# Kernel tuning notes

Measured on AMD Instinct MI355X. Metric: run time of the kernel, lower is better.

The kernel has to match this reference:

```python
import jax, jax.numpy as jnp
import numpy as np

B, S, D = 4, 4096, 256


def setup_inputs() -> dict:
    key = jax.random.key(0)
    ks = jax.random.split(key, 7)
    s = 1.0 / np.sqrt(D)
    return {
        "x": jax.random.normal(ks[0], (B, S, D), dtype=jnp.float32),
        "Wq": jax.random.uniform(ks[1], (D, D), jnp.float32, -s, s),
        "bq": jax.random.uniform(ks[2], (D,), jnp.float32, -s, s),
        "Wk": jax.random.uniform(ks[3], (D, D), jnp.float32, -s, s),
        "bk": jax.random.uniform(ks[4], (D,), jnp.float32, -s, s),
        "Wv": jax.random.uniform(ks[5], (D, D), jnp.float32, -s, s),
        "bv": jax.random.uniform(ks[6], (D,), jnp.float32, -s, s),
    }


def reference(x, Wq, bq, Wk, bk, Wv, bv):
    # nn.Linear: y = x @ W.T + b
    Q = jnp.einsum("bsd,ed->bse", x, Wq) + bq
    K = jnp.einsum("bsd,ed->bse", x, Wk) + bk
    V = jnp.einsum("bsd,ed->bse", x, Wv) + bv
    dk = Q.shape[-1]
    scores = jnp.einsum("bqd,bkd->bqk", Q, K) / jnp.sqrt(jnp.float32(dk))
    # NOTE: original applies softmax over dim=1 (the query axis), not -1.
    attn = jax.nn.softmax(scores, axis=1)
    out = jnp.einsum("bqk,bkd->bqd", attn, V)
    return out
```

## Files before the change

kernel.cpp:

```cpp
#include <hip/hip_runtime.h>

typedef short bf16x8 __attribute__((ext_vector_type(8)));
typedef float f32x4 __attribute__((ext_vector_type(4)));
typedef unsigned short u16;

#define S_LEN 4096
#define D_DIM 256
#define NROW  16384

__device__ __forceinline__ u16 f2bf(float f) {
    union { float f; unsigned u; } v; v.f = f;
    unsigned r = v.u + 0x7FFFu + ((v.u >> 16) & 1u);
    return (u16)(r >> 16);
}
__device__ __forceinline__ float bf2f(u16 h) {
    union { unsigned u; float f; } v; v.u = ((unsigned)h) << 16; return v.f;
}

__device__ __forceinline__ size_t fr_qk(int t, int kk) {
    return (size_t)t * 4096 + kk * 512;
}
__device__ __forceinline__ size_t fr_v(int p, int dt, int kk2) {
    return (size_t)p * 16384 + (dt * 2 + kk2) * 512;
}
__device__ __forceinline__ size_t e_base(int b, int kc, int qt) {
    return ((size_t)(b * 32768 + kc * 256 + qt)) * 512;
}

__device__ __forceinline__ void gll16(const u16* g, u16* l) {
    __builtin_amdgcn_global_load_lds(
        (const __attribute__((address_space(1))) unsigned int*)g,
        (__attribute__((address_space(3))) unsigned int*)l, 16, 0, 0);
}

#define WAITV6 asm volatile("s_waitcnt vmcnt(6)" ::: "memory")
#define WAITV4 asm volatile("s_waitcnt vmcnt(4)" ::: "memory")
#define WAITV0 asm volatile("s_waitcnt vmcnt(0)" ::: "memory")
#define WAITLGKM0 asm volatile("s_waitcnt lgkmcnt(0)" ::: "memory")
#define MEMFENCE asm volatile("" ::: "memory")

__global__ __launch_bounds__(256) void wconv(
    const float* __restrict__ Wq, const float* __restrict__ Wk,
    const float* __restrict__ Wv, u16* __restrict__ Wf)
{
    int i = blockIdx.x * 256 + threadIdx.x;
    int m = i >> 13;
    int idx = i & 8191;
    int ocol = idx >> 5;
    int d0 = (idx & 31) * 8;
    const float* s = (m == 0 ? Wq : (m == 1 ? Wk : Wv)) + ocol * 256 + d0;
    float4 v0 = *reinterpret_cast<const float4*>(s);
    float4 v1 = *reinterpret_cast<const float4*>(s + 4);
    union { ushort4 h[2]; int4 q; } t;
    t.h[0] = make_ushort4(f2bf(v0.x), f2bf(v0.y), f2bf(v0.z), f2bf(v0.w));
    t.h[1] = make_ushort4(f2bf(v1.x), f2bf(v1.y), f2bf(v1.z), f2bf(v1.w));
    size_t off = (size_t)m * 65536 + fr_qk(ocol >> 4, d0 >> 5)
               + ((d0 >> 3) & 3) * 128 + (ocol & 15) * 8;
    *reinterpret_cast<int4*>(Wf + off) = t.q;
}

__global__ __launch_bounds__(256) void qkv_proj(
    const float* __restrict__ x, const u16* __restrict__ Wf,
    const float* __restrict__ bq, const float* __restrict__ bk,
    const float* __restrict__ bv,
    u16* __restrict__ Qf, u16* __restrict__ Kf, u16* __restrict__ Vf)
{
    __shared__ u16 xs[32][264];
    const int tid = threadIdx.x;
    const int r0 = blockIdx.x * 32;

    #pragma unroll
    for (int i = 0; i < 8; ++i) {
        int c = i * 256 + tid;
        int row = c >> 6, c4 = c & 63;
        float4 v = reinterpret_cast<const float4*>(x + (size_t)(r0 + row) * D_DIM)[c4];
        *reinterpret_cast<ushort4*>(&xs[row][c4 * 4]) =
            make_ushort4(f2bf(v.x), f2bf(v.y), f2bf(v.z), f2bf(v.w));
    }
    __syncthreads();

    const int w = tid >> 6, l = tid & 63, lr = l & 15, lg = l >> 4;
    const int c0 = w * 64;

    bf16x8 a[2][8];
    #pragma unroll
    for (int qs = 0; qs < 2; ++qs)
        #pragma unroll
        for (int kk = 0; kk < 8; ++kk)
            a[qs][kk] = *reinterpret_cast<const bf16x8*>(&xs[qs * 16 + lr][kk * 32 + lg * 8]);

    const float* Bs[3] = {bq, bk, bv};

    #pragma unroll
    for (int m = 0; m < 3; ++m) {
        const u16* Wm = Wf + (size_t)m * 65536;
        f32x4 acc[2][4] = {};
        #pragma unroll
        for (int kk = 0; kk < 8; ++kk) {
            #pragma unroll
            for (int cf = 0; cf < 4; ++cf) {
                bf16x8 wfr = *reinterpret_cast<const bf16x8*>(
                    Wm + fr_qk(w * 4 + cf, kk) + l * 8);
                acc[0][cf] = __builtin_amdgcn_mfma_f32_16x16x32_bf16(a[0][kk], wfr, acc[0][cf], 0, 0, 0);
                acc[1][cf] = __builtin_amdgcn_mfma_f32_16x16x32_bf16(a[1][kk], wfr, acc[1][cf], 0, 0, 0);
            }
        }
        if (m < 2) {
            u16* outp = (m == 0) ? Qf : Kf;
            int t = r0 >> 4;
            #pragma unroll
            for (int qs = 0; qs < 2; ++qs) {
                #pragma unroll
                for (int cf = 0; cf < 4; ++cf) {
                    int col = c0 + cf * 16 + lr;
                    float bias = Bs[m][col];
                    size_t base = fr_qk(t + qs, col >> 5) + ((col >> 3) & 3) * 128 + (col & 7);
                    #pragma unroll
                    for (int r = 0; r < 4; ++r)
                        outp[base + (lg * 4 + r) * 8] = f2bf(acc[qs][cf][r] + bias);
                }
            }
        } else {
            int p  = (r0 >> 12) * 64 + ((r0 & 4095) >> 6);
            int kb = r0 & 63;
            #pragma unroll
            for (int qs = 0; qs < 2; ++qs) {
                #pragma unroll
                for (int cf = 0; cf < 4; ++cf) {
                    int d = c0 + cf * 16 + lr;
                    float bias = bv[d];
                    #pragma unroll
                    for (int r = 0; r < 4; ++r) {
                        int key = kb + qs * 16 + lg * 4 + r;
                        size_t off = fr_v(p, d >> 4, key >> 5)
                                   + ((key >> 3) & 3) * 128 + (d & 15) * 8 + (key & 7);
                        Vf[off] = f2bf(acc[qs][cf][r] + bias);
                    }
                }
            }
        }
    }
}

__global__ __launch_bounds__(256, 2) void score_exp(
    const u16* __restrict__ Qf, const u16* __restrict__ Kf,
    u16* __restrict__ Ef, float* __restrict__ Zp, int write_e)
{
    __shared__ __align__(16) u16 Qls[2][8192];
    const int tid = threadIdx.x, blk = blockIdx.x;
    const int xcd = blk & 7, sub = blk >> 3;
    const int b  = xcd >> 1;
    const int qq = ((xcd & 1) << 1) | (sub & 1);
    const int ktile = sub >> 1;
    const int w = tid >> 6, l = tid & 63, lr = l & 15, lg = l >> 4;
    const int k0 = ktile * 128;

    bf16x8 kreg[2][8];
    #pragma unroll
    for (int ks = 0; ks < 2; ++ks) {
        const int tk = b * 256 + (k0 >> 4) + w * 2 + ks;
        #pragma unroll
        for (int kk = 0; kk < 8; ++kk)
            kreg[ks][kk] = *reinterpret_cast<const bf16x8*>(Kf + fr_qk(tk, kk) + l * 8);
    }

    #define STAGE_Q(qt_, nb_) do { \
        const u16* g_ = Qf + ((size_t)(b * 256 + (qt_) * 2)) * 4096 + (w * 4) * 512 + l * 8; \
        u16* d_ = &Qls[nb_][(w * 4) * 512]; \
        _Pragma("unroll") \
        for (int f_ = 0; f_ < 4; ++f_) gll16(g_ + f_ * 512, d_ + f_ * 512); \
    } while (0)

    const int qt0 = qq * 32;
    STAGE_Q(qt0, 0);
    __syncthreads();

    float Z[2][4] = {};
    const float SC = 0.0625f;
    const int kc = ktile * 4 + w;

    for (int it = 0; it < 32; ++it) {
        const int cur = it & 1;
        if (it < 31) STAGE_Q(qt0 + it + 1, cur ^ 1);

        f32x4 acc[2][2] = {};
        #pragma unroll
        for (int kk = 0; kk < 8; ++kk) {
            #pragma unroll
            for (int qf = 0; qf < 2; ++qf) {
                bf16x8 qfr = *reinterpret_cast<const bf16x8*>(
                    &Qls[cur][(qf * 8 + kk) * 512 + l * 8]);
                acc[0][qf] = __builtin_amdgcn_mfma_f32_16x16x32_bf16(kreg[0][kk], qfr, acc[0][qf], 0, 0, 0);
                acc[1][qf] = __builtin_amdgcn_mfma_f32_16x16x32_bf16(kreg[1][kk], qfr, acc[1][qf], 0, 0, 0);
            }
        }
        #pragma unroll
        for (int ks = 0; ks < 2; ++ks) {
            #pragma unroll
            for (int qf = 0; qf < 2; ++qf) {
                float e0 = __expf(acc[ks][qf][0] * SC);
                float e1 = __expf(acc[ks][qf][1] * SC);
                float e2 = __expf(acc[ks][qf][2] * SC);
                float e3 = __expf(acc[ks][qf][3] * SC);
                Z[ks][0] += e0; Z[ks][1] += e1; Z[ks][2] += e2; Z[ks][3] += e3;
                if (write_e) {
                    size_t ad = e_base(b, kc, (qt0 + it) * 2 + qf)
                              + (ks * 2 + (lg >> 1)) * 128 + lr * 8 + (lg & 1) * 4;
                    *reinterpret_cast<ushort4*>(Ef + ad) =
                        make_ushort4(f2bf(e0), f2bf(e1), f2bf(e2), f2bf(e3));
                }
            }
        }
        __syncthreads();
    }

    #pragma unroll
    for (int ks = 0; ks < 2; ++ks) {
        #pragma unroll
        for (int r = 0; r < 4; ++r) {
            float z = Z[ks][r];
            z += __shfl_xor(z, 1);
            z += __shfl_xor(z, 2);
            z += __shfl_xor(z, 4);
            z += __shfl_xor(z, 8);
            if (lr == 0)
                Zp[qq * NROW + b * S_LEN + k0 + w * 32 + ks * 16 + lg * 4 + r] = z;
        }
    }
    #undef STAGE_Q
}

__global__ __launch_bounds__(256) void zrecip(
    const float* __restrict__ Zp, float* __restrict__ rZ)
{
    int i = blockIdx.x * 256 + threadIdx.x;
    rZ[i] = 1.0f / (((Zp[i] + Zp[NROW + i]) + Zp[2 * NROW + i]) + Zp[3 * NROW + i]);
}

__global__ __launch_bounds__(256) void zlog(
    const float* __restrict__ Zp, float* __restrict__ LZ)
{
    int i = blockIdx.x * 256 + threadIdx.x;
    LZ[i] = logf(((Zp[i] + Zp[NROW + i]) + Zp[2 * NROW + i]) + Zp[3 * NROW + i]);
}

__global__ __launch_bounds__(256) void vscale(
    u16* __restrict__ Vf, const float* __restrict__ rZ)
{
    int i = blockIdx.x * 256 + threadIdx.x;
    int frag = i >> 6, l8 = i & 63;
    int p = frag >> 5, sub = frag & 31, kk2 = sub & 1;
    int b = p >> 6, kt = p & 63;
    int kbase = b * S_LEN + kt * 64 + kk2 * 32 + (l8 >> 4) * 8;
    float4 rz0 = *reinterpret_cast<const float4*>(&rZ[kbase]);
    float4 rz1 = *reinterpret_cast<const float4*>(&rZ[kbase + 4]);
    ushort4* vp = reinterpret_cast<ushort4*>(Vf + (size_t)i * 8);
    ushort4 a = vp[0], c = vp[1];
    vp[0] = make_ushort4(f2bf(bf2f(a.x) * rz0.x), f2bf(bf2f(a.y) * rz0.y),
                         f2bf(bf2f(a.z) * rz0.z), f2bf(bf2f(a.w) * rz0.w));
    vp[1] = make_ushort4(f2bf(bf2f(c.x) * rz1.x), f2bf(bf2f(c.y) * rz1.y),
                         f2bf(bf2f(c.z) * rz1.z), f2bf(bf2f(c.w) * rz1.w));
}

__global__ __launch_bounds__(256, 2) void pv_gemm(
    const u16* __restrict__ Ef, const u16* __restrict__ Vf, float* __restrict__ out)
{
    __shared__ __align__(16) u16 Els[3][4096];
    __shared__ __align__(16) u16 Vls[3][8192];

    const int tid = threadIdx.x, blk = blockIdx.x;
    const int xcd = blk & 7, sub = blk >> 3;
    const int b  = xcd >> 1;
    const int kq = ((xcd & 1) << 1) | (sub & 1);
    const int qtile = sub >> 1;
    const int w = tid >> 6, l = tid & 63, lr = l & 15, lg = l >> 4;

    #define STAGE(it_) do { \
        const int kc_ = kq * 32 + (it_); \
        const int nb_ = (it_) % 3; \
        const size_t vb_ = ((size_t)(b * 64 + (kc_ >> 1))) * 16384 + (kc_ & 1) * 512; \
        _Pragma("unroll") \
        for (int i_ = 0; i_ < 6; ++i_) { \
            int f_ = w * 6 + i_; \
            if (f_ < 8) { \
                gll16(Ef + e_base(b, kc_, qtile * 8 + f_) + l * 8, &Els[nb_][f_ * 512]); \
            } else { \
                int dt_ = f_ - 8; \
                gll16(Vf + vb_ + (size_t)dt_ * 1024 + l * 8, &Vls[nb_][dt_ * 512]); \
            } \
        } \
    } while (0)

    STAGE(0);
    STAGE(1);
    WAITV6;
    __builtin_amdgcn_s_barrier();
    MEMFENCE;

    f32x4 acc[2][16] = {};

    #pragma unroll 1
    for (int it = 0; it < 32; ++it) {
        if (it < 30) STAGE(it + 2);
        const int cur = it % 3;
        bf16x8 ef0 = *reinterpret_cast<const bf16x8*>(&Els[cur][(w * 2) * 512 + l * 8]);
        bf16x8 ef1 = *reinterpret_cast<const bf16x8*>(&Els[cur][(w * 2 + 1) * 512 + l * 8]);
        __builtin_amdgcn_s_setprio(1);
        #pragma unroll
        for (int dt = 0; dt < 16; ++dt) {
            bf16x8 vfr = *reinterpret_cast<const bf16x8*>(&Vls[cur][dt * 512 + l * 8]);
            acc[0][dt] = __builtin_amdgcn_mfma_f32_16x16x32_bf16(ef0, vfr, acc[0][dt], 0, 0, 0);
            acc[1][dt] = __builtin_amdgcn_mfma_f32_16x16x32_bf16(ef1, vfr, acc[1][dt], 0, 0, 0);
        }
        __builtin_amdgcn_s_setprio(0);
        if (it < 30) { WAITV6; } else if (it == 30) { WAITV0; }
        if (it < 31) {
            __builtin_amdgcn_s_barrier();
            MEMFENCE;
        }
    }

    const int qg = b * S_LEN + qtile * 128 + w * 32;
    #pragma unroll
    for (int qs = 0; qs < 2; ++qs) {
        #pragma unroll
        for (int dt = 0; dt < 16; ++dt) {
            #pragma unroll
            for (int r = 0; r < 4; ++r) {
                unsafeAtomicAdd(&out[(size_t)(qg + qs * 16 + lg * 4 + r) * D_DIM + dt * 16 + lr],
                                acc[qs][dt][r]);
            }
        }
    }
    #undef STAGE
}

__global__ __launch_bounds__(512, 1) void attn_out_fb(
    const u16* __restrict__ Qf, const u16* __restrict__ Kf, const u16* __restrict__ Vf,
    const float* __restrict__ LZ, float* __restrict__ out)
{
    __shared__ __align__(16) u16 Kls[3][8192];
    __shared__ __align__(16) u16 Vls[4][8192];
    __shared__ __align__(16) u16 ps[8][2][1280];
    __shared__ __align__(16) float lzs[1024];

    const int tid = threadIdx.x, blk = blockIdx.x;
    const int xcd = blk & 7, sub = blk >> 3;
    const int b  = xcd >> 1;
    const int kq = ((xcd & 1) << 1) | (sub & 1);
    const int qtile = sub >> 1;
    const int w = tid >> 6, l = tid & 63, lr = l & 15, lg = l >> 4;
    const int q0 = qtile * 256 + w * 32;
    const int base_tk = b * 256;
    const int kt0 = kq * 32;

    bf16x8 qreg[2][8];
    #pragma unroll
    for (int qs = 0; qs < 2; ++qs) {
        const int tq = base_tk + ((q0 + qs * 16) >> 4);
        #pragma unroll
        for (int kk = 0; kk < 8; ++kk)
            qreg[qs][kk] = *reinterpret_cast<const bf16x8*>(Qf + fr_qk(tq, kk) + l * 8);
    }

    #define STAGE(kt_) do { \
        if (w < 4) { \
            const u16* g_ = Kf + ((size_t)(base_tk + (kt0 + (kt_)) * 2)) * 4096 + (w * 4) * 512 + l * 8; \
            u16* d_ = &Kls[(kt_) % 3][(w * 4) * 512]; \
            _Pragma("unroll") \
            for (int f_ = 0; f_ < 4; ++f_) gll16(g_ + f_ * 512, d_ + f_ * 512); \
        } else { \
            const int kta_ = kt0 + (kt_); \
            const size_t vb_ = ((size_t)(b * 64 + (kta_ >> 1))) * 16384 + (kta_ & 1) * 512; \
            const int dt0_ = (w - 4) * 4; \
            _Pragma("unroll") \
            for (int f_ = 0; f_ < 4; ++f_) \
                gll16(Vf + vb_ + (size_t)(dt0_ + f_) * 1024 + l * 8, &Vls[(kt_) % 4][(dt0_ + f_) * 512]); \
        } \
    } while (0)

    #define QK(kt_) do { \
        const u16* kb_ = &Kls[(kt_) % 3][0]; \
        __builtin_amdgcn_s_setprio(1); \
        _Pragma("unroll") \
        for (int kk = 0; kk < 8; ++kk) { \
            bf16x8 k0_ = *reinterpret_cast<const bf16x8*>(kb_ + kk * 512 + l * 8); \
            bf16x8 k1_ = *reinterpret_cast<const bf16x8*>(kb_ + (8 + kk) * 512 + l * 8); \
            sacc[0][0] = __builtin_amdgcn_mfma_f32_16x16x32_bf16(qreg[0][kk], k0_, sacc[0][0], 0, 0, 0); \
            sacc[0][1] = __builtin_amdgcn_mfma_f32_16x16x32_bf16(qreg[1][kk], k0_, sacc[0][1], 0, 0, 0); \
            sacc[1][0] = __builtin_amdgcn_mfma_f32_16x16x32_bf16(qreg[0][kk], k1_, sacc[1][0], 0, 0, 0); \
            sacc[1][1] = __builtin_amdgcn_mfma_f32_16x16x32_bf16(qreg[1][kk], k1_, sacc[1][1], 0, 0, 0); \
        } \
        __builtin_amdgcn_s_setprio(0); \
    } while (0)

    #define PV(j_) do { \
        const u16* vb_ = &Vls[(j_) % 4][0]; \
        const u16* pb_ = &ps[w][(j_) & 1][0]; \
        bf16x8 af0_ = *reinterpret_cast<const bf16x8*>(pb_ + lr * 40 + lg * 8); \
        bf16x8 af1_ = *reinterpret_cast<const bf16x8*>(pb_ + (16 + lr) * 40 + lg * 8); \
        __builtin_amdgcn_s_setprio(1); \
        _Pragma("unroll") \
        for (int dt = 0; dt < 16; ++dt) { \
            bf16x8 vf_ = *reinterpret_cast<const bf16x8*>(vb_ + dt * 512 + l * 8); \
            oacc[0][dt] = __builtin_amdgcn_mfma_f32_16x16x32_bf16(af0_, vf_, oacc[0][dt], 0, 0, 0); \
            oacc[1][dt] = __builtin_amdgcn_mfma_f32_16x16x32_bf16(af1_, vf_, oacc[1][dt], 0, 0, 0); \
        } \
        __builtin_amdgcn_s_setprio(0); \
    } while (0)

    #define SM(kt_) do { \
        u16* pw_ = &ps[w][(kt_) & 1][0]; \
        _Pragma("unroll") \
        for (int cf = 0; cf < 2; ++cf) { \
            float Lv_ = lzs[(kt_) * 32 + cf * 16 + lr]; \
            _Pragma("unroll") \
            for (int qs = 0; qs < 2; ++qs) \
                _Pragma("unroll") \
                for (int r = 0; r < 4; ++r) { \
                    float p_ = __expf(fmaf(sacc[cf][qs][r], SC, -Lv_)); \
                    pw_[(qs * 16 + lg * 4 + r) * 40 + cf * 16 + lr] = f2bf(p_); \
                } \
        } \
    } while (0)

    f32x4 oacc[2][16] = {};
    const float SC = 0.0625f;

    f32x4 lzv;
    if (tid < 256)
        lzv = *reinterpret_cast<const f32x4*>(LZ + b * S_LEN + kt0 * 32 + tid * 4);
    STAGE(0);
    STAGE(1);
    if (tid < 256)
        *reinterpret_cast<f32x4*>(&lzs[tid * 4]) = lzv;
    WAITLGKM0;
    WAITV4;
    __builtin_amdgcn_s_barrier();
    MEMFENCE;

    #pragma unroll 1
    for (int kt = 0; kt < 30; ++kt) {
        STAGE(kt + 2);
        f32x4 sacc[2][2] = {};
        QK(kt);
        if (kt > 0) PV(kt - 1);
        SM(kt);
        WAITV4;
        __builtin_amdgcn_s_barrier();
        MEMFENCE;
    }
    {
        f32x4 sacc[2][2] = {};
        QK(30); PV(29); SM(30);
        WAITV0;
        __builtin_amdgcn_s_barrier();
        MEMFENCE;
    }
    {
        f32x4 sacc[2][2] = {};
        QK(31); PV(30); SM(31); PV(31);
    }

    #pragma unroll
    for (int qs = 0; qs < 2; ++qs) {
        #pragma unroll
        for (int dt = 0; dt < 16; ++dt) {
            #pragma unroll
            for (int r = 0; r < 4; ++r) {
                int row = q0 + qs * 16 + lg * 4 + r;
                unsafeAtomicAdd(&out[((size_t)(b * S_LEN + row)) * D_DIM + dt * 16 + lr],
                                oacc[qs][dt][r]);
            }
        }
    }
    #undef STAGE
    #undef QK
    #undef PV
    #undef SM
}

extern "C" void kernel_launch(void* const* d_in, const int* in_sizes, int n_in,
                              void* d_out, int out_size, void* d_ws, size_t ws_size,
                              hipStream_t stream) {
    const float* x  = (const float*)d_in[0];
    const float* Wq = (const float*)d_in[1];
    const float* bq = (const float*)d_in[2];
    const float* Wk = (const float*)d_in[3];
    const float* bk = (const float*)d_in[4];
    const float* Wv = (const float*)d_in[5];
    const float* bv = (const float*)d_in[6];
    float* out = (float*)d_out;

    u16* Qf = (u16*)d_ws;
    u16* Kf = Qf + (size_t)NROW * D_DIM;
    u16* Vf = Kf + (size_t)NROW * D_DIM;
    u16* Wf = Vf + (size_t)NROW * D_DIM;
    float* Zp = (float*)(Wf + 196608);
    float* rZ = Zp + 4 * NROW;
    u16* Ef = (u16*)(rZ + NROW);

    const size_t need = (size_t)((char*)Ef - (char*)d_ws) + (size_t)4 * 32768 * 512 * 2;

    hipMemsetAsync(out, 0, (size_t)NROW * D_DIM * sizeof(float), stream);
    wconv<<<96, 256, 0, stream>>>(Wq, Wk, Wv, Wf);
    qkv_proj<<<NROW / 32, 256, 0, stream>>>(x, Wf, bq, bk, bv, Qf, Kf, Vf);

    if (ws_size >= need) {
        score_exp<<<512, 256, 0, stream>>>(Qf, Kf, Ef, Zp, 1);
        zrecip<<<NROW / 256, 256, 0, stream>>>(Zp, rZ);
        vscale<<<2048, 256, 0, stream>>>(Vf, rZ);
        pv_gemm<<<512, 256, 0, stream>>>(Ef, Vf, out);
    } else {
        score_exp<<<512, 256, 0, stream>>>(Qf, Kf, Qf , Zp, 0);
        zlog<<<NROW / 256, 256, 0, stream>>>(Zp, rZ);
        attn_out_fb<<<256, 512, 0, stream>>>(Qf, Kf, Vf, rZ, out);
    }
}
```

Baseline: 169.6 us.

## Retile PV GEMM to 64-query tiles with direct E register loads

The PV GEMM block tile shrinks from 128 queries by 256 dims to 64 queries, with warps split two ways over queries and two ways over dims. The grid doubles to 1024 blocks and the launch bound now targets 4 blocks per SM. E fragments are loaded straight from global into registers instead of through LDS, and V staging drops from triple to double buffering with a full vmcnt(0) wait each step. The goal is higher occupancy and less LDS use, at the cost of reading V twice as often in total and having a shallower prefetch pipeline.

Result: no change. 166.3 us (-1.9%).

```diff
diff --git a/kernel.cpp b/kernel.cpp
--- a/kernel.cpp
+++ b/kernel.cpp
@@ -33,7 +33,6 @@
         (__attribute__((address_space(3))) unsigned int*)l, 16, 0, 0);
 }
 
-#define WAITV6 asm volatile("s_waitcnt vmcnt(6)" ::: "memory")
 #define WAITV4 asm volatile("s_waitcnt vmcnt(4)" ::: "memory")
 #define WAITV0 asm volatile("s_waitcnt vmcnt(0)" ::: "memory")
 #define WAITLGKM0 asm volatile("s_waitcnt lgkmcnt(0)" ::: "memory")
@@ -262,77 +261,97 @@
                          f2bf(bf2f(c.z) * rz1.z), f2bf(bf2f(c.w) * rz1.w));
 }
 
-__global__ __launch_bounds__(256, 2) void pv_gemm(
+__global__ __launch_bounds__(256, 4) void pv_gemm(
     const u16* __restrict__ Ef, const u16* __restrict__ Vf, float* __restrict__ out)
 {
-    __shared__ __align__(16) u16 Els[3][4096];
-    __shared__ __align__(16) u16 Vls[3][8192];
+    __shared__ __align__(16) u16 Vls[2][8192];
 
     const int tid = threadIdx.x, blk = blockIdx.x;
     const int xcd = blk & 7, sub = blk >> 3;
     const int b  = xcd >> 1;
-    const int kq = ((xcd & 1) << 1) | (sub & 1);
-    const int qtile = sub >> 1;
+    const int ks = ((xcd & 1) << 1) | (sub & 1);
+    const int qt64 = sub >> 1;
     const int w = tid >> 6, l = tid & 63, lr = l & 15, lg = l >> 4;
-
-    #define STAGE(it_) do { \
-        const int kc_ = kq * 32 + (it_); \
-        const int nb_ = (it_) % 3; \
+    const int qh = w & 1, dh = w >> 1;
+
+    #define EADDR(it_, j_) \
+        (Ef + e_base(b, ks * 32 + (it_), qt64 * 4 + qh * 2 + (j_)) + l * 8)
+
+    #define STAGE_V(it_, nb_) do { \
+        const int kc_ = ks * 32 + (it_); \
         const size_t vb_ = ((size_t)(b * 64 + (kc_ >> 1))) * 16384 + (kc_ & 1) * 512; \
         _Pragma("unroll") \
-        for (int i_ = 0; i_ < 6; ++i_) { \
-            int f_ = w * 6 + i_; \
-            if (f_ < 8) { \
-                gll16(Ef + e_base(b, kc_, qtile * 8 + f_) + l * 8, &Els[nb_][f_ * 512]); \
-            } else { \
-                int dt_ = f_ - 8; \
-                gll16(Vf + vb_ + (size_t)dt_ * 1024 + l * 8, &Vls[nb_][dt_ * 512]); \
-            } \
+        for (int f_ = 0; f_ < 4; ++f_) { \
+            int dt_ = w * 4 + f_; \
+            gll16(Vf + vb_ + (size_t)(dt_ * 2) * 512 + l * 8, &Vls[nb_][dt_ * 512]); \
         } \
     } while (0)
 
-    STAGE(0);
-    STAGE(1);
-    WAITV6;
+    #define COMPUTE(nb_, e0_, e1_) do { \
+        __builtin_amdgcn_s_setprio(1); \
+        _Pragma("unroll") \
+        for (int dt = 0; dt < 8; ++dt) { \
+            bf16x8 vfr = *reinterpret_cast<const bf16x8*>( \
+                &Vls[nb_][(dh * 8 + dt) * 512 + l * 8]); \
+            acc[0][dt] = __builtin_amdgcn_mfma_f32_16x16x32_bf16(e0_, vfr, acc[0][dt], 0, 0, 0); \
+            acc[1][dt] = __builtin_amdgcn_mfma_f32_16x16x32_bf16(e1_, vfr, acc[1][dt], 0, 0, 0); \
+        } \
+        __builtin_amdgcn_s_setprio(0); \
+    } while (0)
+
+    f32x4 acc[2][8] = {};
+    bf16x8 eA0, eA1, eB0, eB1;
+
+    eA0 = *reinterpret_cast<const bf16x8*>(EADDR(0, 0));
+    eA1 = *reinterpret_cast<const bf16x8*>(EADDR(0, 1));
+    STAGE_V(0, 0);
+    WAITV0;
     __builtin_amdgcn_s_barrier();
     MEMFENCE;
 
-    f32x4 acc[2][16] = {};
-
     #pragma unroll 1
-    for (int it = 0; it < 32; ++it) {
-        if (it < 30) STAGE(it + 2);
-        const int cur = it % 3;
-        bf16x8 ef0 = *reinterpret_cast<const bf16x8*>(&Els[cur][(w * 2) * 512 + l * 8]);
-        bf16x8 ef1 = *reinterpret_cast<const bf16x8*>(&Els[cur][(w * 2 + 1) * 512 + l * 8]);
-        __builtin_amdgcn_s_setprio(1);
-        #pragma unroll
-        for (int dt = 0; dt < 16; ++dt) {
-            bf16x8 vfr = *reinterpret_cast<const bf16x8*>(&Vls[cur][dt * 512 + l * 8]);
-            acc[0][dt] = __builtin_amdgcn_mfma_f32_16x16x32_bf16(ef0, vfr, acc[0][dt], 0, 0, 0);
-            acc[1][dt] = __builtin_amdgcn_mfma_f32_16x16x32_bf16(ef1, vfr, acc[1][dt], 0, 0, 0);
-        }
-        __builtin_amdgcn_s_setprio(0);
-        if (it < 30) { WAITV6; } else if (it == 30) { WAITV0; }
-        if (it < 31) {
-            __builtin_amdgcn_s_barrier();
-            MEMFENCE;
-        }
-    }
-
-    const int qg = b * S_LEN + qtile * 128 + w * 32;
-    #pragma unroll
-    for (int qs = 0; qs < 2; ++qs) {
-        #pragma unroll
-        for (int dt = 0; dt < 16; ++dt) {
+    for (int it = 0; it < 30; it += 2) {
+        eB0 = *reinterpret_cast<const bf16x8*>(EADDR(it + 1, 0));
+        eB1 = *reinterpret_cast<const bf16x8*>(EADDR(it + 1, 1));
+        STAGE_V(it + 1, 1);
+        COMPUTE(0, eA0, eA1);
+        WAITV0;
+        __builtin_amdgcn_s_barrier();
+        MEMFENCE;
+        eA0 = *reinterpret_cast<const bf16x8*>(EADDR(it + 2, 0));
+        eA1 = *reinterpret_cast<const bf16x8*>(EADDR(it + 2, 1));
+        STAGE_V(it + 2, 0);
+        COMPUTE(1, eB0, eB1);
+        WAITV0;
+        __builtin_amdgcn_s_barrier();
+        MEMFENCE;
+    }
+    eB0 = *reinterpret_cast<const bf16x8*>(EADDR(31, 0));
+    eB1 = *reinterpret_cast<const bf16x8*>(EADDR(31, 1));
+    STAGE_V(31, 1);
+    COMPUTE(0, eA0, eA1);
+    WAITV0;
+    __builtin_amdgcn_s_barrier();
+    MEMFENCE;
+    COMPUTE(1, eB0, eB1);
+
+    const int qg = b * S_LEN + qt64 * 64 + qh * 32;
+    const int dg = dh * 128;
+    #pragma unroll
+    for (int qf = 0; qf < 2; ++qf) {
+        #pragma unroll
+        for (int dt = 0; dt < 8; ++dt) {
             #pragma unroll
             for (int r = 0; r < 4; ++r) {
-                unsafeAtomicAdd(&out[(size_t)(qg + qs * 16 + lg * 4 + r) * D_DIM + dt * 16 + lr],
-                                acc[qs][dt][r]);
-            }
-        }
-    }
-    #undef STAGE
+                unsafeAtomicAdd(&out[(size_t)(qg + qf * 16 + lg * 4 + r) * D_DIM
+                                     + dg + dt * 16 + lr],
+                                acc[qf][dt][r]);
+            }
+        }
+    }
+    #undef EADDR
+    #undef STAGE_V
+    #undef COMPUTE
 }
 
 __global__ __launch_bounds__(512, 1) void attn_out_fb(
@@ -510,7 +529,7 @@
         score_exp<<<512, 256, 0, stream>>>(Qf, Kf, Ef, Zp, 1);
         zrecip<<<NROW / 256, 256, 0, stream>>>(Zp, rZ);
         vscale<<<2048, 256, 0, stream>>>(Vf, rZ);
-        pv_gemm<<<512, 256, 0, stream>>>(Ef, Vf, out);
+        pv_gemm<<<1024, 256, 0, stream>>>(Ef, Vf, out);
     } else {
         score_exp<<<512, 256, 0, stream>>>(Qf, Kf, Qf , Zp, 0);
         zlog<<<NROW / 256, 256, 0, stream>>>(Zp, rZ);
```
